# Performance work log

Hardware: AMD Instinct MI355X
Metric: run time of the kernel (lower is better)

## Reference

```python
import jax, jax.numpy as jnp
import numpy as np

HIDDEN, HEADS, HEAD_DIM = 1024, 16, 64
BSZ, SEQ = 2, 2048
SCALE = HEAD_DIM ** (-0.5)
CAUSAL = True


def setup_inputs() -> dict:
    key = jax.random.key(0)
    ks = jax.random.split(key, 7)
    inner = HEADS * HEAD_DIM
    init = lambda k, shape: jax.random.normal(k, shape, dtype=jnp.float32) * (shape[0] ** -0.5)
    return {
        "query": jax.random.normal(ks[0], (BSZ, SEQ, HIDDEN), dtype=jnp.float32),
        "key": jax.random.normal(ks[1], (BSZ, SEQ, HIDDEN), dtype=jnp.float32),
        "value": jax.random.normal(ks[2], (BSZ, SEQ, HIDDEN), dtype=jnp.float32),
        "w_q": init(ks[3], (HIDDEN, inner)),  # stored [in, out]
        "w_k": init(ks[4], (HIDDEN, inner)),
        "w_v": init(ks[5], (HIDDEN, inner)),
        "w_o": init(ks[6], (inner, HIDDEN)),
    }


def reference(query, key, value, w_q, w_k, w_v, w_o):
    bsz, q_len, _ = query.shape
    k_len = key.shape[1]

    def split_heads(x):  # [b, s, h*d] -> [b, h, s, d]
        return x.reshape(x.shape[0], x.shape[1], HEADS, HEAD_DIM).transpose(0, 2, 1, 3)

    q = split_heads(query @ w_q)
    k = split_heads(key @ w_k)
    v = split_heads(value @ w_v)

    scores = jnp.einsum("bhqd,bhkd->bhqk", q, k) * SCALE
    if CAUSAL:
        q_pos = jnp.arange(q_len)
        k_pos = jnp.arange(k_len)
        mask = (k_pos[None, :] <= q_pos[:, None]).astype(scores.dtype)
        scores = scores + (1.0 - mask)[None, None, :, :] * -10000.0
    weights = jax.nn.softmax(scores, axis=-1)
    out = jnp.einsum("bhqk,bhkd->bhqd", weights, v)
    out = out.transpose(0, 2, 1, 3).reshape(bsz, q_len, HEADS * HEAD_DIM)
    return out @ w_o
```

## Files before the change

kernel.cpp:

```cpp
#include <hip/hip_runtime.h>


using u16 = unsigned short;
typedef __bf16 bf16x8 __attribute__((ext_vector_type(8)));
typedef short  s16x8  __attribute__((ext_vector_type(8)));
typedef float  f32x4  __attribute__((ext_vector_type(4)));

#define SEQ   2048
#define QSC   0.18033688f

__device__ __forceinline__ u16 to_bf16(float f) {
  return __builtin_bit_cast(u16, (__bf16)f);
}
__device__ __forceinline__ float from_bf16(u16 v) {
  return __builtin_bit_cast(float, ((unsigned)v) << 16);
}
__device__ __forceinline__ bf16x8 frag_cast(s16x8 v) {
  return __builtin_bit_cast(bf16x8, v);
}
__device__ __forceinline__ f32x4 mfma16(bf16x8 a, bf16x8 b, f32x4 c) {
  return __builtin_amdgcn_mfma_f32_16x16x32_bf16(a, b, c, 0, 0, 0);
}
__device__ __forceinline__ void gload_lds16(const void* g, void* l) {
  __builtin_amdgcn_global_load_lds(
      (const __attribute__((address_space(1))) void*)g,
      (__attribute__((address_space(3))) void*)l, 16, 0, 0);
}

__global__ __launch_bounds__(256) void convert_x(const float* __restrict__ q,
                                                 const float* __restrict__ k,
                                                 const float* __restrict__ v,
                                                 u16* __restrict__ out) {
  const float* src = blockIdx.z == 0 ? q : (blockIdx.z == 1 ? k : v);
  u16* dst = out + (size_t)blockIdx.z * 4194304;
  for (int idx = blockIdx.x * 256 + threadIdx.x; idx < 524288; idx += 512 * 256) {
    const float4* p = (const float4*)(src + (size_t)idx * 8);
    float4 a = p[0], b = p[1];
    s16x8 o;
    o[0] = (short)to_bf16(a.x); o[1] = (short)to_bf16(a.y);
    o[2] = (short)to_bf16(a.z); o[3] = (short)to_bf16(a.w);
    o[4] = (short)to_bf16(b.x); o[5] = (short)to_bf16(b.y);
    o[6] = (short)to_bf16(b.z); o[7] = (short)to_bf16(b.w);
    *(s16x8*)(dst + (size_t)idx * 8) = o;
  }
}

__global__ __launch_bounds__(256) void transpose_w(const float* __restrict__ wq,
                                                   const float* __restrict__ wk,
                                                   const float* __restrict__ wv,
                                                   const float* __restrict__ wo,
                                                   u16* __restrict__ wT) {
  __shared__ float tile[32][33];
  const float* src = blockIdx.z == 0 ? wq : blockIdx.z == 1 ? wk
                     : blockIdx.z == 2 ? wv : wo;
  u16* dst = wT + (size_t)blockIdx.z * 1048576;
  const int x0 = blockIdx.x * 32, y0 = blockIdx.y * 32;
  const int tx = threadIdx.x, ty = threadIdx.y;
#pragma unroll
  for (int i = 0; i < 4; ++i)
    tile[ty + i * 8][tx] = src[(size_t)(y0 + ty + i * 8) * 1024 + x0 + tx];
  __syncthreads();
#pragma unroll
  for (int i = 0; i < 4; ++i)
    dst[(size_t)(x0 + ty + i * 8) * 1024 + y0 + tx] = to_bf16(tile[tx][ty + i * 8]);
}

__global__ __launch_bounds__(256) void gemm_qkv(const u16* __restrict__ X,
                                                const u16* __restrict__ WT,
                                                u16* __restrict__ Qb,
                                                u16* __restrict__ Kb,
                                                u16* __restrict__ VTb) {
  __shared__ u16 As[128 * 32];
  __shared__ u16 Bs[128 * 32];
  const int z = blockIdx.z;
  const u16* A = X + (size_t)z * 4194304;
  const u16* BT = WT + (size_t)z * 1048576;
  const int tid = threadIdx.x;
  const int w = tid >> 6, lane = tid & 63;
  const int g = lane >> 4, c = lane & 15;
  const int wr = w >> 1, wc = w & 1;
  const int row0 = blockIdx.x * 128;
  const int n0 = blockIdx.y * 128;

  f32x4 acc[4][4];
#pragma unroll
  for (int i = 0; i < 4; ++i)
#pragma unroll
    for (int j = 0; j < 4; ++j) acc[i][j] = (f32x4){0.f, 0.f, 0.f, 0.f};

  const int sub = lane >> 2;
  const int kk = (lane & 3) * 8;

  for (int kt = 0; kt < 32; ++kt) {
    const int k0 = kt * 32;
#pragma unroll
    for (int it = 0; it < 2; ++it) {
      const int ch = w * 2 + it;
      const int row = ch * 16 + sub;
      gload_lds16(A + (size_t)(row0 + row) * 1024 + k0 + kk, (char*)As + ch * 1024);
      gload_lds16(BT + (size_t)(n0 + row) * 1024 + k0 + kk, (char*)Bs + ch * 1024);
    }
    __syncthreads();

    bf16x8 af[4], bfr[4];
#pragma unroll
    for (int mi = 0; mi < 4; ++mi)
      af[mi] = frag_cast(*(const s16x8*)((const char*)As + (wr * 64 + mi * 16 + c) * 64 + g * 16));
#pragma unroll
    for (int ni = 0; ni < 4; ++ni)
      bfr[ni] = frag_cast(*(const s16x8*)((const char*)Bs + (wc * 64 + ni * 16 + c) * 64 + g * 16));
#pragma unroll
    for (int mi = 0; mi < 4; ++mi)
#pragma unroll
      for (int ni = 0; ni < 4; ++ni)
        acc[mi][ni] = mfma16(af[mi], bfr[ni], acc[mi][ni]);
    __syncthreads();
  }

  const float sc = (z == 0) ? QSC : 1.0f;
#pragma unroll
  for (int mi = 0; mi < 4; ++mi) {
    const int rowb = row0 + wr * 64 + mi * 16 + g * 4;
#pragma unroll
    for (int ni = 0; ni < 4; ++ni) {
      const int col = n0 + wc * 64 + ni * 16 + c;
#pragma unroll
      for (int r = 0; r < 4; ++r) {
        const int row = rowb + r;
        const float v = acc[mi][ni][r] * sc;
        if (z == 2) {
          const int b = row >> 11, s = row & 2047;
          const int hh = col >> 6, d = col & 63;
          VTb[((size_t)((b * 16 + hh) * 64 + d)) * 2048 + s] = to_bf16(v);
        } else {
          u16* C = z == 0 ? Qb : Kb;
          C[(size_t)row * 1024 + col] = to_bf16(v);
        }
      }
    }
  }
}

__global__ __launch_bounds__(256) void gemm_out(const u16* __restrict__ A,
                                                const u16* __restrict__ BT,
                                                float* __restrict__ C) {
  __shared__ u16 As[64 * 32];
  __shared__ u16 Bs[128 * 32];
  const int tid = threadIdx.x;
  const int w = tid >> 6, lane = tid & 63;
  const int g = lane >> 4, c = lane & 15;
  const int wr = w >> 1, wc = w & 1;
  const int row0 = blockIdx.x * 64;
  const int n0 = blockIdx.y * 128;

  f32x4 acc[2][4];
#pragma unroll
  for (int i = 0; i < 2; ++i)
#pragma unroll
    for (int j = 0; j < 4; ++j) acc[i][j] = (f32x4){0.f, 0.f, 0.f, 0.f};

  const int sub = lane >> 2;
  const int kk = (lane & 3) * 8;

  for (int kt = 0; kt < 32; ++kt) {
    const int k0 = kt * 32;
    {
      const int row = w * 16 + sub;
      gload_lds16(A + (size_t)(row0 + row) * 1024 + k0 + kk, (char*)As + w * 1024);
    }
#pragma unroll
    for (int it = 0; it < 2; ++it) {
      const int ch = w * 2 + it;
      const int row = ch * 16 + sub;
      gload_lds16(BT + (size_t)(n0 + row) * 1024 + k0 + kk, (char*)Bs + ch * 1024);
    }
    __syncthreads();

    bf16x8 af[2], bfr[4];
#pragma unroll
    for (int mi = 0; mi < 2; ++mi)
      af[mi] = frag_cast(*(const s16x8*)((const char*)As + (wr * 32 + mi * 16 + c) * 64 + g * 16));
#pragma unroll
    for (int ni = 0; ni < 4; ++ni)
      bfr[ni] = frag_cast(*(const s16x8*)((const char*)Bs + (wc * 64 + ni * 16 + c) * 64 + g * 16));
#pragma unroll
    for (int mi = 0; mi < 2; ++mi)
#pragma unroll
      for (int ni = 0; ni < 4; ++ni)
        acc[mi][ni] = mfma16(af[mi], bfr[ni], acc[mi][ni]);
    __syncthreads();
  }

#pragma unroll
  for (int mi = 0; mi < 2; ++mi) {
    const int rowb = row0 + wr * 32 + mi * 16 + g * 4;
#pragma unroll
    for (int ni = 0; ni < 4; ++ni) {
      const int col = n0 + wc * 64 + ni * 16 + c;
#pragma unroll
      for (int r = 0; r < 4; ++r)
        C[(size_t)(rowb + r) * 1024 + col] = acc[mi][ni][r];
    }
  }
}

__global__ __launch_bounds__(512, 8) void attn_fwd(const u16* __restrict__ Qb,
                                                   const u16* __restrict__ Kb,
                                                   const u16* __restrict__ VTb,
                                                   u16* __restrict__ PO,
                                                   float* __restrict__ ML) {
  __shared__ u16 Ks[2][64 * 64];
  __shared__ u16 VTs[2][64 * 64];

  const int tid = threadIdx.x;
  const int w = tid >> 6, lane = tid & 63;
  const int g = lane >> 4, c = lane & 15;
  const int bh = blockIdx.y;
  const int b = bh >> 4, h = bh & 15;

  int sid = blockIdx.x, x = 0;
  for (; x < 16; ++x) {
    const int ns_ = (2 * x + 9) >> 3;
    if (sid < ns_) break;
    sid -= ns_;
  }
  const int ns = (2 * x + 9) >> 3;
  const int n = 2 * x + 2;
  const int t0 = (sid * n) / ns, t1 = ((sid + 1) * n) / ns;
  const int sg = blockIdx.x + 40 * bh;
  const int q0w = x * 128 + w * 16;

  bf16x8 qfr[2];
#pragma unroll
  for (int ch = 0; ch < 2; ++ch)
    qfr[ch] = frag_cast(*(const s16x8*)(Qb + (size_t)(b * SEQ + q0w + c) * 1024 + h * 64 + ch * 32 + g * 8));

  f32x4 oacc[4];
#pragma unroll
  for (int j = 0; j < 4; ++j) oacc[j] = (f32x4){0.f, 0.f, 0.f, 0.f};
  float m_run = -1e30f;
  float l_run = 0.f;

  const int srow = tid >> 3;
  const int scol = (tid & 7) * 8;
  const int prow = (srow & 35) | ((srow & 4) << 2) | ((srow & 24) >> 1);
  const int ksw = prow * 128 + ((scol * 2) ^ ((prow & 7) << 4));
  const int vsw = srow * 128 + ((scol * 2) ^ ((srow & 7) << 4));

  s16x8 kreg, vreg;
#define LOADKV(T)                                                                            \
  {                                                                                          \
    const int kv0_ = (T)*64;                                                                 \
    kreg = *(const s16x8*)(Kb + (size_t)(b * SEQ + kv0_ + srow) * 1024 + h * 64 + scol);     \
    vreg = *(const s16x8*)(VTb + ((size_t)(bh * 64 + srow)) * 2048 + kv0_ + scol);           \
  }
#define WRITEKV(BUF)                                                                         \
  {                                                                                          \
    *(s16x8*)((char*)Ks[BUF] + ksw) = kreg;                                                  \
    *(s16x8*)((char*)VTs[BUF] + vsw) = vreg;                                                 \
  }

  LOADKV(t0);
  WRITEKV(0);
  __syncthreads();

  int cur = 0;
  for (int t = t0; t < t1; ++t) {
    const bool pre = (t + 1 < t1);
    if (pre) LOADKV(t + 1);

    const bool skip = (t * 64 > q0w + 15);
    if (!skip) {
      f32x4 sa[4];
#pragma unroll
      for (int i = 0; i < 4; ++i) sa[i] = (f32x4){0.f, 0.f, 0.f, 0.f};
#pragma unroll
      for (int kvf = 0; kvf < 4; ++kvf) {
        const int kr = kvf * 16 + c;
        const int rb = kr * 128, swz = (kr & 7) << 4;
#pragma unroll
        for (int ch = 0; ch < 2; ++ch) {
          const bf16x8 ak = frag_cast(*(const s16x8*)((char*)Ks[cur] + rb + ((ch * 64 + g * 16) ^ swz)));
          sa[kvf] = mfma16(ak, qfr[ch], sa[kvf]);
        }
      }

      float pv[4][4];
      float mt = -1e30f;
      if (t * 64 + 63 > q0w) {
        const int q_abs = q0w + c;
#pragma unroll
        for (int kvf = 0; kvf < 4; ++kvf) {
          const int kvb = t * 64 + (kvf >> 1) * 32 + (kvf & 1) * 4 + 8 * g;
#pragma unroll
          for (int r = 0; r < 4; ++r) {
            float s = sa[kvf][r];
            if (kvb + r > q_abs) s = -30000.f;
            pv[kvf][r] = s;
            mt = fmaxf(mt, s);
          }
        }
      } else {
#pragma unroll
        for (int kvf = 0; kvf < 4; ++kvf)
#pragma unroll
          for (int r = 0; r < 4; ++r) {
            const float s = sa[kvf][r];
            pv[kvf][r] = s;
            mt = fmaxf(mt, s);
          }
      }
      mt = fmaxf(mt, __shfl_xor(mt, 16));
      mt = fmaxf(mt, __shfl_xor(mt, 32));

      if (__any(mt > m_run + 8.f)) {
        const float m_new = fmaxf(m_run, mt);
        const float alpha = __builtin_amdgcn_exp2f(m_run - m_new);
        m_run = m_new;
#pragma unroll
        for (int r = 0; r < 4; ++r) {
          const float ar = __shfl(alpha, g * 4 + r);
#pragma unroll
          for (int df = 0; df < 4; ++df) oacc[df][r] *= ar;
        }
        l_run *= alpha;
      }

      float ls = 0.f;
      s16x8 pk[2];
#pragma unroll
      for (int kvf = 0; kvf < 4; ++kvf)
#pragma unroll
        for (int r = 0; r < 4; ++r) {
          const float p = __builtin_amdgcn_exp2f(pv[kvf][r] - m_run);
          ls += p;
          pk[kvf >> 1][(kvf & 1) * 4 + r] = (short)to_bf16(p);
        }
      ls += __shfl_xor(ls, 16);
      ls += __shfl_xor(ls, 32);
      l_run += ls;

#pragma unroll
      for (int ch = 0; ch < 2; ++ch) {
        const bf16x8 ap = frag_cast(pk[ch]);
#pragma unroll
        for (int df = 0; df < 4; ++df) {
          const int dr = df * 16 + c;
          const bf16x8 bv = frag_cast(*(const s16x8*)((char*)VTs[cur] + dr * 128 +
                                                      ((ch * 64 + g * 16) ^ ((dr & 7) << 4))));
          oacc[df] = mfma16(ap, bv, oacc[df]);
        }
      }
    }

    if (pre) WRITEKV(cur ^ 1);
    __syncthreads();
    cur ^= 1;
  }

  const size_t pob = (size_t)sg * 8192;
#pragma unroll
  for (int r = 0; r < 4; ++r) {
    const int row = w * 16 + g * 4 + r;
#pragma unroll
    for (int df = 0; df < 4; ++df)
      PO[pob + row * 64 + df * 16 + c] = to_bf16(oacc[df][r]);
  }
  if (g == 0) {
    ML[sg * 256 + (w * 16 + c) * 2 + 0] = m_run;
    ML[sg * 256 + (w * 16 + c) * 2 + 1] = l_run;
  }
}

__global__ __launch_bounds__(512) void attn_merge(const u16* __restrict__ PO,
                                                  const float* __restrict__ ML,
                                                  u16* __restrict__ Ob) {
  const int x = blockIdx.x, bh = blockIdx.y;
  const int b = bh >> 4, h = bh & 15;
  const int tid = threadIdx.x;
  const int row = tid >> 2, c0 = (tid & 3) << 4;

  int base = 0;
  for (int xp = 0; xp < x; ++xp) base += (2 * xp + 9) >> 3;
  const int ns = (2 * x + 9) >> 3;
  const int sg0 = base + 40 * bh;

  float m[4], l[4], a[4];
  float M = -3e38f;
  for (int i = 0; i < ns; ++i) {
    m[i] = ML[(sg0 + i) * 256 + row * 2 + 0];
    l[i] = ML[(sg0 + i) * 256 + row * 2 + 1];
    M = fmaxf(M, m[i]);
  }
  float denom = 0.f;
  for (int i = 0; i < ns; ++i) {
    a[i] = __builtin_amdgcn_exp2f(m[i] - M);
    denom += a[i] * l[i];
  }
  const float inv = 1.f / denom;

  float o[16];
#pragma unroll
  for (int j = 0; j < 16; ++j) o[j] = 0.f;
  for (int i = 0; i < ns; ++i) {
    const float s = a[i] * inv;
    const u16* p = PO + (size_t)(sg0 + i) * 8192 + row * 64 + c0;
    const s16x8 v0 = *(const s16x8*)p;
    const s16x8 v1 = *(const s16x8*)(p + 8);
#pragma unroll
    for (int j = 0; j < 8; ++j) {
      o[j] += s * from_bf16((u16)v0[j]);
      o[8 + j] += s * from_bf16((u16)v1[j]);
    }
  }

  s16x8 lo, hi;
#pragma unroll
  for (int j = 0; j < 8; ++j) {
    lo[j] = (short)to_bf16(o[j]);
    hi[j] = (short)to_bf16(o[8 + j]);
  }
  u16* dst = Ob + (size_t)(b * SEQ + x * 128 + row) * 1024 + h * 64 + c0;
  *(s16x8*)dst = lo;
  *(s16x8*)(dst + 8) = hi;
}

extern "C" void kernel_launch(void* const* d_in, const int* in_sizes, int n_in,
                              void* d_out, int out_size, void* d_ws, size_t ws_size,
                              hipStream_t stream) {
  const float* query = (const float*)d_in[0];
  const float* key_ = (const float*)d_in[1];
  const float* value = (const float*)d_in[2];
  const float* w_q = (const float*)d_in[3];
  const float* w_k = (const float*)d_in[4];
  const float* w_v = (const float*)d_in[5];
  const float* w_o = (const float*)d_in[6];

  char* ws = (char*)d_ws;
  u16* xq = (u16*)(ws + 0);
  u16* PO = (u16*)(ws + 0);
  u16* wT = (u16*)(ws + 25165824);
  float* ML = (float*)(ws + 25165824);
  u16* Qb = (u16*)(ws + 33554432);
  u16* Kb = (u16*)(ws + 41943040);
  u16* VTb = (u16*)(ws + 50331648);
  u16* Ob = (u16*)(ws + 58720256);

  convert_x<<<dim3(512, 1, 3), 256, 0, stream>>>(query, key_, value, xq);
  transpose_w<<<dim3(32, 32, 4), dim3(32, 8), 0, stream>>>(w_q, w_k, w_v, w_o, wT);
  gemm_qkv<<<dim3(32, 8, 3), 256, 0, stream>>>(xq, wT, Qb, Kb, VTb);
  attn_fwd<<<dim3(40, 32), 512, 0, stream>>>(Qb, Kb, VTb, PO, ML);
  attn_merge<<<dim3(16, 32), 512, 0, stream>>>(PO, ML, Ob);
  gemm_out<<<dim3(64, 8), 256, 0, stream>>>(Ob, wT + 3145728, (float*)d_out);
}
```

Baseline: 133.8 us.

## Use 128-wide KV tiles, MFMA row-sum, and XCD-aware block remapping in attention

```diff
diff --git a/kernel.cpp b/kernel.cpp
--- a/kernel.cpp
+++ b/kernel.cpp
@@ -204,30 +204,34 @@
   }
 }
 
-__global__ __launch_bounds__(512, 8) void attn_fwd(const u16* __restrict__ Qb,
+__global__ __launch_bounds__(512, 4) void attn_fwd(const u16* __restrict__ Qb,
                                                    const u16* __restrict__ Kb,
                                                    const u16* __restrict__ VTb,
                                                    u16* __restrict__ PO,
                                                    float* __restrict__ ML) {
-  __shared__ u16 Ks[2][64 * 64];
-  __shared__ u16 VTs[2][64 * 64];
+  __shared__ u16 Ks[2][128 * 64];
+  __shared__ u16 VTs[2][64 * 128];
 
   const int tid = threadIdx.x;
   const int w = tid >> 6, lane = tid & 63;
   const int g = lane >> 4, c = lane & 15;
-  const int bh = blockIdx.y;
+
+  const int flat = blockIdx.x + 40 * blockIdx.y;
+  const int logical = (flat & 7) * 160 + (flat >> 3);
+  const int slice_id = logical % 40;
+  const int bh = logical / 40;
   const int b = bh >> 4, h = bh & 15;
 
-  int sid = blockIdx.x, x = 0;
+  int sid = slice_id, x = 0;
   for (; x < 16; ++x) {
-    const int ns_ = (2 * x + 9) >> 3;
+    const int ns_ = (x + 4) >> 2;
     if (sid < ns_) break;
     sid -= ns_;
   }
-  const int ns = (2 * x + 9) >> 3;
-  const int n = 2 * x + 2;
-  const int t0 = (sid * n) / ns, t1 = ((sid + 1) * n) / ns;
-  const int sg = blockIdx.x + 40 * bh;
+  const int ns = (x + 4) >> 2;
+  const int np = x + 1;
+  const int t0 = (sid * np) / ns, t1 = ((sid + 1) * np) / ns;
+  const int sg = slice_id + 40 * bh;
   const int q0w = x * 128 + w * 16;
 
   bf16x8 qfr[2];
@@ -235,29 +239,42 @@
   for (int ch = 0; ch < 2; ++ch)
     qfr[ch] = frag_cast(*(const s16x8*)(Qb + (size_t)(b * SEQ + q0w + c) * 1024 + h * 64 + ch * 32 + g * 8));
 
+  s16x8 ones_s;
+#pragma unroll
+  for (int j = 0; j < 8; ++j) ones_s[j] = (short)0x3F80;
+  const bf16x8 onesf = frag_cast(ones_s);
+
   f32x4 oacc[4];
 #pragma unroll
   for (int j = 0; j < 4; ++j) oacc[j] = (f32x4){0.f, 0.f, 0.f, 0.f};
+  f32x4 lacc = (f32x4){0.f, 0.f, 0.f, 0.f};
   float m_run = -1e30f;
-  float l_run = 0.f;
 
   const int srow = tid >> 3;
   const int scol = (tid & 7) * 8;
-  const int prow = (srow & 35) | ((srow & 4) << 2) | ((srow & 24) >> 1);
-  const int ksw = prow * 128 + ((scol * 2) ^ ((prow & 7) << 4));
-  const int vsw = srow * 128 + ((scol * 2) ^ ((srow & 7) << 4));
-
-  s16x8 kreg, vreg;
-#define LOADKV(T)                                                                            \
-  {                                                                                          \
-    const int kv0_ = (T)*64;                                                                 \
-    kreg = *(const s16x8*)(Kb + (size_t)(b * SEQ + kv0_ + srow) * 1024 + h * 64 + scol);     \
-    vreg = *(const s16x8*)(VTb + ((size_t)(bh * 64 + srow)) * 2048 + kv0_ + scol);           \
-  }
-#define WRITEKV(BUF)                                                                         \
-  {                                                                                          \
-    *(s16x8*)((char*)Ks[BUF] + ksw) = kreg;                                                  \
-    *(s16x8*)((char*)VTs[BUF] + vsw) = vreg;                                                 \
+  const int vd = tid >> 4;
+  const int vcol = (tid & 15) * 8;
+
+  s16x8 kreg[2], vreg[2];
+#define LOADKV(T)                                                                              \
+  {                                                                                            \
+    const int kv0_ = (T)*128;                                                                  \
+    _Pragma("unroll") for (int it = 0; it < 2; ++it) {                                         \
+      kreg[it] = *(const s16x8*)(Kb + (size_t)(b * SEQ + kv0_ + srow + it * 64) * 1024 +       \
+                                 h * 64 + scol);                                               \
+      vreg[it] = *(const s16x8*)(VTb + ((size_t)(bh * 64 + vd + it * 32)) * 2048 + kv0_ +      \
+                                 vcol);                                                        \
+    }                                                                                          \
+  }
+#define WRITEKV(BUF)                                                                           \
+  {                                                                                            \
+    _Pragma("unroll") for (int it = 0; it < 2; ++it) {                                         \
+      const int rr_ = srow + it * 64;                                                          \
+      const int pr_ = (rr_ & 0x63) | ((rr_ & 4) << 2) | ((rr_ & 0x18) >> 1);                   \
+      *(s16x8*)((char*)Ks[BUF] + pr_ * 128 + ((scol * 2) ^ ((pr_ & 7) << 4))) = kreg[it];      \
+      const int vr_ = vd + it * 32;                                                            \
+      *(s16x8*)((char*)VTs[BUF] + vr_ * 256 + ((vcol * 2) ^ ((vr_ & 7) << 4))) = vreg[it];     \
+    }                                                                                          \
   }
 
   LOADKV(t0);
@@ -269,13 +286,13 @@
     const bool pre = (t + 1 < t1);
     if (pre) LOADKV(t + 1);
 
-    const bool skip = (t * 64 > q0w + 15);
-    if (!skip) {
-      f32x4 sa[4];
-#pragma unroll
-      for (int i = 0; i < 4; ++i) sa[i] = (f32x4){0.f, 0.f, 0.f, 0.f};
-#pragma unroll
-      for (int kvf = 0; kvf < 4; ++kvf) {
+    const int kv0 = t * 128;
+    if (!(kv0 > q0w + 15)) {
+      f32x4 sa[8];
+#pragma unroll
+      for (int i = 0; i < 8; ++i) sa[i] = (f32x4){0.f, 0.f, 0.f, 0.f};
+#pragma unroll
+      for (int kvf = 0; kvf < 8; ++kvf) {
         const int kr = kvf * 16 + c;
         const int rb = kr * 128, swz = (kr & 7) << 4;
 #pragma unroll
@@ -285,30 +302,25 @@
         }
       }
 
-      float pv[4][4];
       float mt = -1e30f;
-      if (t * 64 + 63 > q0w) {
+      if (kv0 + 127 > q0w) {
         const int q_abs = q0w + c;
 #pragma unroll
-        for (int kvf = 0; kvf < 4; ++kvf) {
-          const int kvb = t * 64 + (kvf >> 1) * 32 + (kvf & 1) * 4 + 8 * g;
+        for (int kvf = 0; kvf < 8; ++kvf) {
+          const int kvb = kv0 + (kvf >> 1) * 32 + (kvf & 1) * 4 + 8 * g;
 #pragma unroll
           for (int r = 0; r < 4; ++r) {
             float s = sa[kvf][r];
             if (kvb + r > q_abs) s = -30000.f;
-            pv[kvf][r] = s;
+            sa[kvf][r] = s;
             mt = fmaxf(mt, s);
           }
         }
       } else {
 #pragma unroll
-        for (int kvf = 0; kvf < 4; ++kvf)
-#pragma unroll
-          for (int r = 0; r < 4; ++r) {
-            const float s = sa[kvf][r];
-            pv[kvf][r] = s;
-            mt = fmaxf(mt, s);
-          }
+        for (int kvf = 0; kvf < 8; ++kvf)
+#pragma unroll
+          for (int r = 0; r < 4; ++r) mt = fmaxf(mt, sa[kvf][r]);
       }
       mt = fmaxf(mt, __shfl_xor(mt, 16));
       mt = fmaxf(mt, __shfl_xor(mt, 32));
@@ -322,34 +334,30 @@
           const float ar = __shfl(alpha, g * 4 + r);
 #pragma unroll
           for (int df = 0; df < 4; ++df) oacc[df][r] *= ar;
-        }
-        l_run *= alpha;
+          lacc[r] *= ar;
+        }
       }
 
-      float ls = 0.f;
-      s16x8 pk[2];
-#pragma unroll
-      for (int kvf = 0; kvf < 4; ++kvf)
+      s16x8 pk[4];
+#pragma unroll
+      for (int kvf = 0; kvf < 8; ++kvf)
 #pragma unroll
         for (int r = 0; r < 4; ++r) {
-          const float p = __builtin_amdgcn_exp2f(pv[kvf][r] - m_run);
-          ls += p;
+          const float p = __builtin_amdgcn_exp2f(sa[kvf][r] - m_run);
           pk[kvf >> 1][(kvf & 1) * 4 + r] = (short)to_bf16(p);
         }
-      ls += __shfl_xor(ls, 16);
-      ls += __shfl_xor(ls, 32);
-      l_run += ls;
-
-#pragma unroll
-      for (int ch = 0; ch < 2; ++ch) {
+
+#pragma unroll
+      for (int ch = 0; ch < 4; ++ch) {
         const bf16x8 ap = frag_cast(pk[ch]);
 #pragma unroll
         for (int df = 0; df < 4; ++df) {
           const int dr = df * 16 + c;
-          const bf16x8 bv = frag_cast(*(const s16x8*)((char*)VTs[cur] + dr * 128 +
+          const bf16x8 bv = frag_cast(*(const s16x8*)((char*)VTs[cur] + dr * 256 +
                                                       ((ch * 64 + g * 16) ^ ((dr & 7) << 4))));
           oacc[df] = mfma16(ap, bv, oacc[df]);
         }
+        lacc = mfma16(ap, onesf, lacc);
       }
     }
 
@@ -366,9 +374,12 @@
     for (int df = 0; df < 4; ++df)
       PO[pob + row * 64 + df * 16 + c] = to_bf16(oacc[df][r]);
   }
-  if (g == 0) {
+  if (g == 0)
     ML[sg * 256 + (w * 16 + c) * 2 + 0] = m_run;
-    ML[sg * 256 + (w * 16 + c) * 2 + 1] = l_run;
+  if (c == 0) {
+#pragma unroll
+    for (int r = 0; r < 4; ++r)
+      ML[sg * 256 + (w * 16 + g * 4 + r) * 2 + 1] = lacc[r];
   }
 }
 
@@ -381,8 +392,8 @@
   const int row = tid >> 2, c0 = (tid & 3) << 4;
 
   int base = 0;
-  for (int xp = 0; xp < x; ++xp) base += (2 * xp + 9) >> 3;
-  const int ns = (2 * x + 9) >> 3;
+  for (int xp = 0; xp < x; ++xp) base += (xp + 4) >> 2;
+  const int ns = (x + 4) >> 2;
   const int sg0 = base + 40 * bh;
 
   float m[4], l[4], a[4];
```

Measured after the change: 121.7 us. 9.0% less time.
